# Optimization experiments

Hardware: AMD Instinct MI355X
Metric: run time of the kernel (lower is better)

## Reference

```python
import jax, jax.numpy as jnp
import numpy as np

EMBED_DIM = 1024
NUM_HEADS = 16
HEAD_DIM = EMBED_DIM // NUM_HEADS
B, N = 4, 2048
EPS = 1e-5


def rotate_half(x):
    x2d = x.reshape(x.shape[:-1] + (-1, 2))
    x1, x2 = x2d[..., 0], x2d[..., 1]
    return jnp.stack([-x2, x1], axis=-1).reshape(x.shape)


def apply_rotary_emb(freqs, t):
    return t * freqs[0] + rotate_half(t) * freqs[1]


def setup_inputs() -> dict:
    key = jax.random.key(0)
    ks = jax.random.split(key, 12)
    d = EMBED_DIM
    inp = {
        "x": jax.random.normal(ks[0], (B, N, d), jnp.float32),
        "encoding": jax.random.normal(ks[1], (2, N, HEAD_DIM), jnp.float32),
        "Wqkv_w": jax.random.normal(ks[2], (d, 3 * d), jnp.float32) * (1.0 / np.sqrt(d)),
        "Wqkv_b": jnp.zeros((3 * d,), jnp.float32),
        "out_w": jax.random.normal(ks[3], (d, d), jnp.float32) * (1.0 / np.sqrt(d)),
        "out_b": jnp.zeros((d,), jnp.float32),
        "ffn0_w": jax.random.normal(ks[4], (2 * d, 2 * d), jnp.float32) * (1.0 / np.sqrt(2 * d)),
        "ffn0_b": jnp.zeros((2 * d,), jnp.float32),
        "ln_scale": jnp.ones((2 * d,), jnp.float32),
        "ln_bias": jnp.zeros((2 * d,), jnp.float32),
        "ffn3_w": jax.random.normal(ks[5], (2 * d, d), jnp.float32) * (1.0 / np.sqrt(2 * d)),
        "ffn3_b": jnp.zeros((d,), jnp.float32),
    }
    return inp


def reference(x, encoding, Wqkv_w, Wqkv_b, out_w, out_b, ffn0_w, ffn0_b, ln_scale, ln_bias, ffn3_w, ffn3_b):
    b, n, d = x.shape
    # fused QKV projection
    qkv = jnp.einsum('bnd,de->bne', x, Wqkv_w) + Wqkv_b
    qkv = qkv.reshape(b, n, NUM_HEADS, HEAD_DIM, 3).transpose(0, 2, 1, 3, 4)  # (b,h,n,hd,3)
    q, k, v = qkv[..., 0], qkv[..., 1], qkv[..., 2]
    # RoPE (encoding broadcasts over batch/heads)
    q = apply_rotary_emb(encoding, q)
    k = apply_rotary_emb(encoding, k)
    # attention (no mask)
    scale = 1.0 / jnp.sqrt(jnp.asarray(HEAD_DIM, x.dtype))
    logits = jnp.einsum('bhqd,bhkd->bhqk', q, k) * scale
    attn = jax.nn.softmax(logits, axis=-1)
    context = jnp.einsum('bhqk,bhkd->bhqd', attn, v)
    message = context.transpose(0, 2, 1, 3).reshape(b, n, d)
    message = jnp.einsum('bnd,de->bne', message, out_w) + out_b
    # FFN: concat -> Dense -> LayerNorm -> GELU(exact) -> Dense
    h = jnp.concatenate([x, message], axis=-1)
    h = jnp.einsum('bnd,de->bne', h, ffn0_w) + ffn0_b
    mu = jnp.mean(h, axis=-1, keepdims=True)
    var = jnp.mean(jnp.square(h - mu), axis=-1, keepdims=True)
    h = (h - mu) * jax.lax.rsqrt(var + EPS) * ln_scale + ln_bias
    h = jax.nn.gelu(h, approximate=False)
    res = jnp.einsum('bnd,de->bne', h, ffn3_w) + ffn3_b
    return x + res
```

## Files before the change

### kernel.cpp

```cpp
#include <hip/hip_runtime.h>
#include <hip/hip_bf16.h>
#include <math.h>

typedef __bf16 bf16x8 __attribute__((ext_vector_type(8)));
typedef float f32x4 __attribute__((ext_vector_type(4)));

#define MFMA16(a, b, c) __builtin_amdgcn_mfma_f32_16x16x32_bf16((a), (b), (c), 0, 0, 0)

__device__ __forceinline__ void gload16(const void* g, void* l) {
  __builtin_amdgcn_global_load_lds((const __attribute__((address_space(1))) void*)g,
                                   (__attribute__((address_space(3))) void*)l, 16, 0, 0);
}

#define BARRIER asm volatile("s_barrier" ::: "memory")

__global__ __launch_bounds__(256) void transpose_bf16(const float* __restrict__ in,
                                                      int ldin,
                                                      __bf16* __restrict__ out,
                                                      int ldo) {
  __shared__ float tile[32][33];
  int n0 = blockIdx.x * 32, k0 = blockIdx.y * 32;
  int tx = threadIdx.x & 31, ty = threadIdx.x >> 5;
#pragma unroll
  for (int r = 0; r < 32; r += 8)
    tile[ty + r][tx] = in[(size_t)(k0 + ty + r) * ldin + n0 + tx];
  __syncthreads();
#pragma unroll
  for (int r = 0; r < 32; r += 8)
    out[(size_t)(n0 + ty + r) * ldo + k0 + tx] = (__bf16)tile[tx][ty + r];
}

__global__ __launch_bounds__(256) void transpose_qkv_perm(const float* __restrict__ in,
                                                          __bf16* __restrict__ out) {
  __shared__ float tile[32][33];
  int n0 = blockIdx.x * 32, k0 = blockIdx.y * 32;
  int tx = threadIdx.x & 31, ty = threadIdx.x >> 5;
#pragma unroll
  for (int r = 0; r < 32; r += 8)
    tile[ty + r][tx] = in[(size_t)(k0 + ty + r) * 3072 + n0 + tx];
  __syncthreads();
#pragma unroll
  for (int r = 0; r < 32; r += 8) {
    int n = n0 + ty + r;
    int h = n / 192, rem = n % 192, hd = rem / 3, which = rem % 3;
    int np = which * 1024 + h * 64 + hd;
    out[(size_t)np * 1024 + k0 + tx] = (__bf16)tile[tx][ty + r];
  }
}

__global__ __launch_bounds__(256) void bias_perm(const float* __restrict__ b,
                                                 float* __restrict__ bp) {
  int n = blockIdx.x * 256 + threadIdx.x;
  if (n < 3072) {
    int h = n / 192, rem = n % 192, hd = rem / 3, which = rem % 3;
    bp[which * 1024 + h * 64 + hd] = b[n];
  }
}

__global__ __launch_bounds__(256) void convert_plain(const float* __restrict__ in,
                                                     __bf16* __restrict__ out) {
  int id = blockIdx.x * 256 + threadIdx.x;
  const float* src = in + (size_t)id * 8;
  __bf16 tmp[8];
#pragma unroll
  for (int e = 0; e < 8; ++e) tmp[e] = (__bf16)src[e];
  *(uint4*)(out + (size_t)id * 8) = *(uint4*)tmp;
}

__global__ __launch_bounds__(256) void convert_x(const float* __restrict__ x,
                                                 __bf16* __restrict__ h) {
  int id = blockIdx.x * 256 + threadIdx.x;
  int row = id >> 7, cc = id & 127;
  const float* src = x + (size_t)row * 1024 + cc * 8;
  __bf16 tmp[8];
#pragma unroll
  for (int e = 0; e < 8; ++e) tmp[e] = (__bf16)src[e];
  *(uint4*)(h + (size_t)row * 2048 + cc * 8) = *(uint4*)tmp;
}

__global__ __launch_bounds__(256) void fuse_bias_part(const float* __restrict__ bout,
                                                      const float* __restrict__ w0,
                                                      float* __restrict__ part) {
  int n = blockIdx.x * 256 + threadIdx.x;
  int e0 = blockIdx.y * 64;
  float s = 0.f;
#pragma unroll 4
  for (int e = 0; e < 64; ++e)
    s += bout[e0 + e] * w0[(size_t)(1024 + e0 + e) * 2048 + n];
  part[(size_t)blockIdx.y * 2048 + n] = s;
}

__global__ __launch_bounds__(256) void fuse_bias_red(const float* __restrict__ part,
                                                     const float* __restrict__ b0,
                                                     float* __restrict__ bf) {
  int n = blockIdx.x * 256 + threadIdx.x;
  float s = b0[n];
#pragma unroll
  for (int y = 0; y < 16; ++y) s += part[(size_t)y * 2048 + n];
  bf[n] = s;
}

template <typename OutT, bool HAS_RES, bool HAS_BIAS>
__global__ __launch_bounds__(256) void gemm_kernel(
    const __bf16* __restrict__ A, int lda,
    const __bf16* __restrict__ Bt,
    const float* __restrict__ bias,
    OutT* __restrict__ C, int ldc,
    const float* __restrict__ res,
    int M, int Nn, int K) {
  __shared__ __attribute__((aligned(16))) __bf16 As[128 * 64];
  __shared__ __attribute__((aligned(16))) __bf16 Bs[128 * 64];

  const int t = threadIdx.x;
  const int row0A = blockIdx.x * 128;
  const int row0B = blockIdx.y * 128;
  const int wave = t >> 6, lane = t & 63;
  const int wm = wave >> 1, wn = wave & 1;
  const int g = lane >> 4, lr = lane & 15;

  f32x4 acc[4][4] = {};

  for (int k0 = 0; k0 < K; k0 += 64) {
#pragma unroll
    for (int p = 0; p < 4; ++p) {
      int cbase = (wave * 4 + p) * 64;
      int ci = cbase + lane;
      int r = ci >> 3, cp = ci & 7, cl = cp ^ (r & 7);
      gload16(A + (size_t)(row0A + r) * lda + k0 + cl * 8, &As[cbase * 8]);
      gload16(Bt + (size_t)(row0B + r) * K + k0 + cl * 8, &Bs[cbase * 8]);
    }
    __syncthreads();
#pragma unroll
    for (int kk = 0; kk < 2; ++kk) {
      bf16x8 af[4], bfr[4];
#pragma unroll
      for (int mt = 0; mt < 4; ++mt) {
        int r = wm * 64 + mt * 16 + lr, c = kk * 4 + g;
        af[mt] = *(const bf16x8*)((char*)As + r * 128 + ((c ^ (r & 7)) * 16));
      }
#pragma unroll
      for (int nt = 0; nt < 4; ++nt) {
        int r = wn * 64 + nt * 16 + lr, c = kk * 4 + g;
        bfr[nt] = *(const bf16x8*)((char*)Bs + r * 128 + ((c ^ (r & 7)) * 16));
      }
#pragma unroll
      for (int mt = 0; mt < 4; ++mt)
#pragma unroll
        for (int nt = 0; nt < 4; ++nt)
          acc[mt][nt] = MFMA16(af[mt], bfr[nt], acc[mt][nt]);
    }
    __syncthreads();
  }

  float bias_v[4];
#pragma unroll
  for (int nt = 0; nt < 4; ++nt)
    bias_v[nt] = HAS_BIAS ? bias[row0B + wn * 64 + nt * 16 + lr] : 0.f;
#pragma unroll
  for (int mt = 0; mt < 4; ++mt) {
    int grow_base = row0A + wm * 64 + mt * 16 + g * 4;
#pragma unroll
    for (int nt = 0; nt < 4; ++nt) {
      int gcol = row0B + wn * 64 + nt * 16 + lr;
#pragma unroll
      for (int j = 0; j < 4; ++j) {
        int grow = grow_base + j;
        float v = acc[mt][nt][j] + bias_v[nt];
        if (HAS_RES) v += res[(size_t)grow * ldc + gcol];
        C[(size_t)grow * ldc + gcol] = (OutT)v;
      }
    }
  }
}

template <typename OutT>
__global__ __launch_bounds__(512, 2) void gemm256p(
    const __bf16* __restrict__ A, int lda,
    const __bf16* __restrict__ Bt, int ldb,
    const float* __restrict__ bias,
    OutT* __restrict__ C, int ldc, int K) {
  __shared__ __attribute__((aligned(16))) __bf16 As[2][256 * 64];
  __shared__ __attribute__((aligned(16))) __bf16 Bs[2][256 * 64];

  const int t = threadIdx.x;
  const int wave = t >> 6, lane = t & 63;
  const int wm = wave >> 2, wn = wave & 3;
  const int g = lane >> 4, lr = lane & 15;
  const int row0A = blockIdx.x * 256, row0B = blockIdx.y * 256;
  const int L = K >> 6;

  f32x4 acc[8][4] = {};

#define STG_A(tile, i)                                                        \
  {                                                                           \
    int cb = ((i) * 8 + wave) * 64;                                           \
    int ci = cb + lane;                                                       \
    int r = ci >> 3, cl = (ci & 7) ^ (r & 7);                                 \
    gload16(A + (size_t)(row0A + r) * lda + (size_t)(tile) * 64 + cl * 8,     \
            &As[(tile) & 1][cb * 8]);                                         \
  }
#define STG_B(tile, i)                                                        \
  {                                                                           \
    int cb = ((i) * 8 + wave) * 64;                                           \
    int ci = cb + lane;                                                       \
    int r = ci >> 3, cl = (ci & 7) ^ (r & 7);                                 \
    gload16(Bt + (size_t)(row0B + r) * ldb + (size_t)(tile) * 64 + cl * 8,    \
            &Bs[(tile) & 1][cb * 8]);                                         \
  }
#define AFRAG(d, mi, ks)                                                      \
  (*(const bf16x8*)((const char*)As[d] + (wm * 128 + (mi) * 16 + lr) * 128 +  \
                    ((((ks) * 4 + g) ^ (lr & 7)) * 16)))
#define BFRAG(d, ni, ks)                                                      \
  (*(const bf16x8*)((const char*)Bs[d] + (wn * 64 + (ni) * 16 + lr) * 128 +   \
                    ((((ks) * 4 + g) ^ (lr & 7)) * 16)))

#pragma unroll
  for (int i = 0; i < 4; ++i) STG_A(0, i);
#pragma unroll
  for (int i = 0; i < 4; ++i) STG_B(0, i);
  STG_A(1, 0);
  STG_A(1, 1);
  asm volatile("s_waitcnt vmcnt(2)" ::: "memory");
  BARRIER;

  for (int tt = 0; tt < L; ++tt) {
    const int d = tt & 1;
    const bool s1 = (tt + 1) < L, s2 = (tt + 2) < L;
    bf16x8 aL[4][2], aH[4][2], bL[2][2], bH[2][2];

#pragma unroll
    for (int mi = 0; mi < 4; ++mi) {
      aL[mi][0] = AFRAG(d, mi, 0);
      aL[mi][1] = AFRAG(d, mi, 1);
    }
#pragma unroll
    for (int ni = 0; ni < 2; ++ni) {
      bL[ni][0] = BFRAG(d, ni, 0);
      bL[ni][1] = BFRAG(d, ni, 1);
    }
    if (s1) { STG_A(tt + 1, 2); STG_A(tt + 1, 3); }
    BARRIER;
    __builtin_amdgcn_s_setprio(1);
#pragma unroll
    for (int mi = 0; mi < 4; ++mi)
#pragma unroll
      for (int ni = 0; ni < 2; ++ni) {
        acc[mi][ni] = MFMA16(aL[mi][0], bL[ni][0], acc[mi][ni]);
        acc[mi][ni] = MFMA16(aL[mi][1], bL[ni][1], acc[mi][ni]);
      }
    __builtin_amdgcn_s_setprio(0);
    BARRIER;

#pragma unroll
    for (int ni = 0; ni < 2; ++ni) {
      bH[ni][0] = BFRAG(d, ni + 2, 0);
      bH[ni][1] = BFRAG(d, ni + 2, 1);
    }
    if (s1) { STG_B(tt + 1, 0); STG_B(tt + 1, 1); }
    BARRIER;
    __builtin_amdgcn_s_setprio(1);
#pragma unroll
    for (int mi = 0; mi < 4; ++mi)
#pragma unroll
      for (int ni = 0; ni < 2; ++ni) {
        acc[mi][ni + 2] = MFMA16(aL[mi][0], bH[ni][0], acc[mi][ni + 2]);
        acc[mi][ni + 2] = MFMA16(aL[mi][1], bH[ni][1], acc[mi][ni + 2]);
      }
    __builtin_amdgcn_s_setprio(0);
    BARRIER;

#pragma unroll
    for (int mi = 0; mi < 4; ++mi) {
      aH[mi][0] = AFRAG(d, mi + 4, 0);
      aH[mi][1] = AFRAG(d, mi + 4, 1);
    }
    if (s1) { STG_B(tt + 1, 2); STG_B(tt + 1, 3); }
    BARRIER;
    __builtin_amdgcn_s_setprio(1);
#pragma unroll
    for (int mi = 0; mi < 4; ++mi)
#pragma unroll
      for (int ni = 0; ni < 2; ++ni) {
        acc[mi + 4][ni + 2] = MFMA16(aH[mi][0], bH[ni][0], acc[mi + 4][ni + 2]);
        acc[mi + 4][ni + 2] = MFMA16(aH[mi][1], bH[ni][1], acc[mi + 4][ni + 2]);
      }
    __builtin_amdgcn_s_setprio(0);
    BARRIER;

    if (s2) { STG_A(tt + 2, 0); STG_A(tt + 2, 1); }
    __builtin_amdgcn_s_setprio(1);
#pragma unroll
    for (int mi = 0; mi < 4; ++mi)
#pragma unroll
      for (int ni = 0; ni < 2; ++ni) {
        acc[mi + 4][ni] = MFMA16(aH[mi][0], bL[ni][0], acc[mi + 4][ni]);
        acc[mi + 4][ni] = MFMA16(aH[mi][1], bL[ni][1], acc[mi + 4][ni]);
      }
    __builtin_amdgcn_s_setprio(0);
    if (s2)
      asm volatile("s_waitcnt vmcnt(2)" ::: "memory");
    else
      asm volatile("s_waitcnt vmcnt(0)" ::: "memory");
    BARRIER;
  }
#undef STG_A
#undef STG_B
#undef AFRAG
#undef BFRAG

  float bias_v[4];
#pragma unroll
  for (int ni = 0; ni < 4; ++ni) bias_v[ni] = bias[row0B + wn * 64 + ni * 16 + lr];
#pragma unroll
  for (int mi = 0; mi < 8; ++mi) {
    int grow_base = row0A + wm * 128 + mi * 16 + g * 4;
#pragma unroll
    for (int ni = 0; ni < 4; ++ni) {
      int gcol = row0B + wn * 64 + ni * 16 + lr;
#pragma unroll
      for (int j = 0; j < 4; ++j)
        C[(size_t)(grow_base + j) * ldc + gcol] = (OutT)(acc[mi][ni][j] + bias_v[ni]);
    }
  }
}

__global__ __launch_bounds__(256) void rope_scatter(
    const __bf16* __restrict__ qkv, const float* __restrict__ enc,
    __bf16* __restrict__ q, __bf16* __restrict__ kk, __bf16* __restrict__ vt) {
  int bh = blockIdx.y;
  int b = bh >> 4, h = bh & 15;
  int n0 = blockIdx.x * 64;
  int t = threadIdx.x;
  const float QSC = 0.125f * 1.44269504088896f;
#pragma unroll
  for (int i = 0; i < 2; ++i) {
    int id = t + i * 256;
    int nl = id >> 3, cc = id & 7;
    int n = n0 + nl;
    size_t row = (size_t)(b * 2048 + n) * 3072;
    bf16x8 qv = *(const bf16x8*)(qkv + row + h * 64 + cc * 8);
    bf16x8 kv = *(const bf16x8*)(qkv + row + 1024 + h * 64 + cc * 8);
    const float* e0 = enc + (size_t)n * 64 + cc * 8;
    const float* e1 = e0 + 131072;
    __bf16 qo[8], ko[8];
#pragma unroll
    for (int e = 0; e < 8; e += 2) {
      float q0 = (float)qv[e], q1 = (float)qv[e + 1];
      float k0 = (float)kv[e], k1 = (float)kv[e + 1];
      float f00 = e0[e], f01 = e0[e + 1], f10 = e1[e], f11 = e1[e + 1];
      qo[e] = (__bf16)((q0 * f00 - q1 * f10) * QSC);
      qo[e + 1] = (__bf16)((q1 * f01 + q0 * f11) * QSC);
      ko[e] = (__bf16)(k0 * f00 - k1 * f10);
      ko[e + 1] = (__bf16)(k1 * f01 + k0 * f11);
    }
    size_t qb = ((size_t)bh * 2048 + n) * 64 + cc * 8;
    *(uint4*)(q + qb) = *(uint4*)qo;
    *(uint4*)(kk + qb) = *(uint4*)ko;
  }
#pragma unroll
  for (int i = 0; i < 2; ++i) {
    int id = t + i * 256;
    int hd = id >> 3, c = id & 7;
    __bf16 tmp[8];
#pragma unroll
    for (int e = 0; e < 8; ++e) {
      int kv = (c >> 2) * 32 + (e >> 2) * 16 + (c & 3) * 4 + (e & 3);
      int n = n0 + kv;
      tmp[e] = qkv[(size_t)(b * 2048 + n) * 3072 + 2048 + h * 64 + hd];
    }
    *(uint4*)(vt + ((size_t)bh * 64 + hd) * 2048 + n0 + c * 8) = *(uint4*)tmp;
  }
}

__global__ __launch_bounds__(256) void attn_kernel(
    const __bf16* __restrict__ q, const __bf16* __restrict__ k,
    const __bf16* __restrict__ vt, __bf16* __restrict__ ctx) {
  __shared__ __attribute__((aligned(16))) __bf16 Ks[2][64 * 64];
  __shared__ __attribute__((aligned(16))) __bf16 Vs[2][64 * 64];

  int nwg = gridDim.x * gridDim.y;
  int bid0 = blockIdx.y * gridDim.x + blockIdx.x;
  int bid = (bid0 & 7) * (nwg >> 3) + (bid0 >> 3);
  const int bh = bid >> 4, qblk = bid & 15;
  const int b = bh >> 4, h = bh & 15;
  const int q0 = qblk * 128;
  const int t = threadIdx.x, wave = t >> 6, lane = t & 63;
  const int g = lane >> 4, lr = lane & 15;
  const int qrow0 = q0 + wave * 32;

  const __bf16* kbase = k + (size_t)bh * 2048 * 64;
  const __bf16* vbase = vt + (size_t)bh * 64 * 2048;

  bf16x8 qf[2][2];
#pragma unroll
  for (int u = 0; u < 2; ++u)
#pragma unroll
    for (int kc = 0; kc < 2; ++kc)
      qf[u][kc] = *(const bf16x8*)(q + ((size_t)bh * 2048 + qrow0 + u * 16 + lr) * 64 +
                                   kc * 32 + g * 8);

  bf16x8 ones;
#pragma unroll
  for (int e = 0; e < 8; ++e) ones[e] = (__bf16)1.0f;

  f32x4 o[2][4] = {};
  f32x4 lacc[2] = {};

#define STAGE_ATTN(buf, kv0)                                                    \
  {                                                                             \
    _Pragma("unroll") for (int p = 0; p < 2; ++p) {                             \
      int cbase = wave * 128 + p * 64;                                          \
      int ci = cbase + lane;                                                    \
      int r = ci >> 3, cp = ci & 7, cl = cp ^ (r & 7);                          \
      gload16(kbase + (size_t)((kv0) + r) * 64 + cl * 8, &Ks[buf][cbase * 8]);  \
      gload16(vbase + (size_t)r * 2048 + (kv0) + cl * 8, &Vs[buf][cbase * 8]);  \
    }                                                                           \
  }

  STAGE_ATTN(0, 0);
  __syncthreads();
  int buf = 0;

  for (int kv0 = 0; kv0 < 2048; kv0 += 64) {
    if (kv0 + 64 < 2048) STAGE_ATTN(buf ^ 1, kv0 + 64);

    f32x4 s[2][4];
    __builtin_amdgcn_s_setprio(1);
#pragma unroll
    for (int nt = 0; nt < 4; ++nt) {
      int r = nt * 16 + lr;
      bf16x8 kf0 = *(const bf16x8*)((char*)Ks[buf] + r * 128 + ((g ^ (r & 7)) * 16));
      bf16x8 kf1 = *(const bf16x8*)((char*)Ks[buf] + r * 128 + (((4 + g) ^ (r & 7)) * 16));
#pragma unroll
      for (int u = 0; u < 2; ++u) {
        f32x4 a = {};
        a = MFMA16(kf0, qf[u][0], a);
        a = MFMA16(kf1, qf[u][1], a);
        s[u][nt] = a;
      }
    }
    __builtin_amdgcn_s_setprio(0);

#pragma unroll
    for (int t2 = 0; t2 < 2; ++t2) {
      bf16x8 pf[2];
#pragma unroll
      for (int u = 0; u < 2; ++u) {
#pragma unroll
        for (int e = 0; e < 8; ++e)
          pf[u][e] = (__bf16)__builtin_amdgcn_exp2f(s[u][2 * t2 + (e >> 2)][e & 3]);
        lacc[u] = MFMA16(ones, pf[u], lacc[u]);
      }
      __builtin_amdgcn_s_setprio(1);
#pragma unroll
      for (int nt = 0; nt < 4; ++nt) {
        int r = nt * 16 + lr;
        bf16x8 vf = *(const bf16x8*)((char*)Vs[buf] + r * 128 + (((t2 * 4 + g) ^ (r & 7)) * 16));
#pragma unroll
        for (int u = 0; u < 2; ++u) o[u][nt] = MFMA16(vf, pf[u], o[u][nt]);
      }
      __builtin_amdgcn_s_setprio(0);
    }
    __syncthreads();
    buf ^= 1;
  }

#pragma unroll
  for (int u = 0; u < 2; ++u) {
    float inv = 1.f / lacc[u][0];
    size_t obase = ((size_t)(b * 2048 + qrow0 + u * 16 + lr)) * 2048 + 1024 + h * 64;
#pragma unroll
    for (int nt = 0; nt < 4; ++nt) {
      __bf16 w4[4];
#pragma unroll
      for (int j = 0; j < 4; ++j) w4[j] = (__bf16)(o[u][nt][j] * inv);
      *(uint2*)(ctx + obase + nt * 16 + g * 4) = *(uint2*)w4;
    }
  }
#undef STAGE_ATTN
}

__global__ __launch_bounds__(256) void ln_gelu(const __bf16* __restrict__ hin,
                                               const float* __restrict__ lns,
                                               const float* __restrict__ lnb,
                                               __bf16* __restrict__ hout) {
  int row = blockIdx.x;
  const __bf16* rp = hin + (size_t)row * 2048;
  int t = threadIdx.x;
  __bf16 tmp[8];
  *(uint4*)tmp = *(const uint4*)(rp + t * 8);
  float vals[8], s = 0.f, s2 = 0.f;
#pragma unroll
  for (int e = 0; e < 8; ++e) {
    float x = (float)tmp[e];
    vals[e] = x;
    s += x;
    s2 += x * x;
  }
#pragma unroll
  for (int m = 1; m < 64; m <<= 1) {
    s += __shfl_xor(s, m, 64);
    s2 += __shfl_xor(s2, m, 64);
  }
  __shared__ float red[8];
  int wave = t >> 6, lane = t & 63;
  if (lane == 0) { red[wave] = s; red[4 + wave] = s2; }
  __syncthreads();
  s = red[0] + red[1] + red[2] + red[3];
  s2 = red[4] + red[5] + red[6] + red[7];
  float mu = s * (1.f / 2048.f);
  float var = s2 * (1.f / 2048.f) - mu * mu;
  float rstd = rsqrtf(var + 1e-5f);
  __bf16 outv[8];
#pragma unroll
  for (int e = 0; e < 8; ++e) {
    int c = t * 8 + e;
    float xh = (vals[e] - mu) * rstd * lns[c] + lnb[c];
    float gg = 0.5f * xh * (1.f + erff(xh * 0.70710678118f));
    outv[e] = (__bf16)gg;
  }
  *(uint4*)(hout + (size_t)row * 2048 + t * 8) = *(uint4*)outv;
}

extern "C" void kernel_launch(void* const* d_in, const int* in_sizes, int n_in,
                              void* d_out, int out_size, void* d_ws, size_t ws_size,
                              hipStream_t stream) {
  const float* x = (const float*)d_in[0];
  const float* enc = (const float*)d_in[1];
  const float* wqkv = (const float*)d_in[2];
  const float* bqkv = (const float*)d_in[3];
  const float* wout = (const float*)d_in[4];
  const float* bout = (const float*)d_in[5];
  const float* wffn0 = (const float*)d_in[6];
  const float* bffn0 = (const float*)d_in[7];
  const float* lns = (const float*)d_in[8];
  const float* lnb = (const float*)d_in[9];
  const float* wffn3 = (const float*)d_in[10];
  const float* bffn3 = (const float*)d_in[11];
  float* out = (float*)d_out;
  char* ws = (char*)d_ws;

  __bf16* wT_qkv = (__bf16*)(ws + 0);
  __bf16* wT_ffn0 = (__bf16*)(ws + 6291456);
  __bf16* wT_ffn3 = (__bf16*)(ws + 14680064);
  __bf16* wout_bf = (__bf16*)(ws + 18874368);
  __bf16* w0bT = (__bf16*)(ws + 20971520);
  float* bias_part = (float*)(ws + 20971520);
  float* bqkv_p = (float*)(ws + 25165824);
  float* bffn0_f = (float*)(ws + 25178112);
  __bf16* h_in = (__bf16*)(ws + 25186304);
  __bf16* qkv = (__bf16*)(ws + 58740736);
  __bf16* ffn0o = qkv;
  __bf16* qb = (__bf16*)(ws + 109072384);
  __bf16* h2 = qb;
  __bf16* kb = (__bf16*)(ws + 125849600);
  __bf16* vtb = (__bf16*)(ws + 142626816);

  dim3 blk(256);
  transpose_qkv_perm<<<dim3(96, 32), blk, 0, stream>>>(wqkv, wT_qkv);
  bias_perm<<<12, blk, 0, stream>>>(bqkv, bqkv_p);
  transpose_bf16<<<dim3(64, 32), blk, 0, stream>>>(wffn0, 2048, wT_ffn0, 2048);
  transpose_bf16<<<dim3(64, 32), blk, 0, stream>>>(wffn0 + (size_t)1024 * 2048, 2048,
                                                   w0bT, 1024);
  transpose_bf16<<<dim3(32, 64), blk, 0, stream>>>(wffn3, 1024, wT_ffn3, 2048);
  convert_plain<<<512, blk, 0, stream>>>(wout, wout_bf);
  gemm_kernel<__bf16, false, false><<<dim3(16, 8), blk, 0, stream>>>(
      w0bT, 1024, wout_bf, nullptr, wT_ffn0 + 1024, 2048, nullptr, 2048, 1024, 1024);
  fuse_bias_part<<<dim3(8, 16), blk, 0, stream>>>(bout, wffn0, bias_part);
  fuse_bias_red<<<8, blk, 0, stream>>>(bias_part, bffn0, bffn0_f);
  convert_x<<<4096, blk, 0, stream>>>(x, h_in);

  gemm256p<__bf16><<<dim3(32, 12), dim3(512), 0, stream>>>(
      h_in, 2048, wT_qkv, 1024, bqkv_p, qkv, 3072, 1024);

  rope_scatter<<<dim3(32, 64), blk, 0, stream>>>(qkv, enc, qb, kb, vtb);
  attn_kernel<<<dim3(16, 64), blk, 0, stream>>>(qb, kb, vtb, h_in);

  gemm256p<__bf16><<<dim3(32, 8), dim3(512), 0, stream>>>(
      h_in, 2048, wT_ffn0, 2048, bffn0_f, ffn0o, 2048, 2048);

  ln_gelu<<<8192, blk, 0, stream>>>(ffn0o, lns, lnb, h2);

  gemm_kernel<float, true, true><<<dim3(64, 8), blk, 0, stream>>>(
      h2, 2048, wT_ffn3, bffn3, out, 1024, x, 8192, 1024, 2048);
}
```

Measured before the change: 393.7 us.

## Merge prep kernels into two launches and double attention query tile per wave

Ten weight/bias/input preparation kernels are collapsed into two launches (prep1 dispatching by block index, prep2 combining the wout-fold GEMM with the bias reduction). This cuts launch overhead and inter-kernel gaps, and bias_part moves to its own workspace slot so it no longer aliases w0bT. The attention kernel now handles 256 query rows per block (64 per wave), which halves the grid and reuses each staged K/V tile across twice as many queries. The cost is more registers for the o, lacc and pf accumulators, which may lower occupancy.

```diff
diff --git a/kernel.cpp b/kernel.cpp
--- a/kernel.cpp
+++ b/kernel.cpp
@@ -14,13 +14,10 @@
 
 #define BARRIER asm volatile("s_barrier" ::: "memory")
 
-__global__ __launch_bounds__(256) void transpose_bf16(const float* __restrict__ in,
-                                                      int ldin,
-                                                      __bf16* __restrict__ out,
-                                                      int ldo) {
-  __shared__ float tile[32][33];
-  int n0 = blockIdx.x * 32, k0 = blockIdx.y * 32;
-  int tx = threadIdx.x & 31, ty = threadIdx.x >> 5;
+__device__ __forceinline__ void tr_body(float (*tile)[33], const float* __restrict__ in,
+                                        int ldin, __bf16* __restrict__ out, int ldo,
+                                        int n0, int k0, int t) {
+  int tx = t & 31, ty = t >> 5;
 #pragma unroll
   for (int r = 0; r < 32; r += 8)
     tile[ty + r][tx] = in[(size_t)(k0 + ty + r) * ldin + n0 + tx];
@@ -30,74 +27,141 @@
     out[(size_t)(n0 + ty + r) * ldo + k0 + tx] = (__bf16)tile[tx][ty + r];
 }
 
-__global__ __launch_bounds__(256) void transpose_qkv_perm(const float* __restrict__ in,
-                                                          __bf16* __restrict__ out) {
+__global__ __launch_bounds__(256) void prep1(
+    const float* __restrict__ wqkv, __bf16* __restrict__ wT_qkv,
+    const float* __restrict__ wffn0, __bf16* __restrict__ wT_ffn0,
+    __bf16* __restrict__ w0bT,
+    const float* __restrict__ wffn3, __bf16* __restrict__ wT_ffn3,
+    const float* __restrict__ wout, __bf16* __restrict__ wout_bf,
+    const float* __restrict__ bqkv, float* __restrict__ bqkv_p,
+    const float* __restrict__ bout, float* __restrict__ bias_part,
+    const float* __restrict__ x, __bf16* __restrict__ h_in) {
   __shared__ float tile[32][33];
-  int n0 = blockIdx.x * 32, k0 = blockIdx.y * 32;
-  int tx = threadIdx.x & 31, ty = threadIdx.x >> 5;
-#pragma unroll
-  for (int r = 0; r < 32; r += 8)
-    tile[ty + r][tx] = in[(size_t)(k0 + ty + r) * 3072 + n0 + tx];
-  __syncthreads();
-#pragma unroll
-  for (int r = 0; r < 32; r += 8) {
-    int n = n0 + ty + r;
-    int h = n / 192, rem = n % 192, hd = rem / 3, which = rem % 3;
-    int np = which * 1024 + h * 64 + hd;
-    out[(size_t)np * 1024 + k0 + tx] = (__bf16)tile[tx][ty + r];
-  }
-}
-
-__global__ __launch_bounds__(256) void bias_perm(const float* __restrict__ b,
-                                                 float* __restrict__ bp) {
-  int n = blockIdx.x * 256 + threadIdx.x;
-  if (n < 3072) {
-    int h = n / 192, rem = n % 192, hd = rem / 3, which = rem % 3;
-    bp[which * 1024 + h * 64 + hd] = b[n];
-  }
-}
-
-__global__ __launch_bounds__(256) void convert_plain(const float* __restrict__ in,
-                                                     __bf16* __restrict__ out) {
-  int id = blockIdx.x * 256 + threadIdx.x;
-  const float* src = in + (size_t)id * 8;
-  __bf16 tmp[8];
-#pragma unroll
-  for (int e = 0; e < 8; ++e) tmp[e] = (__bf16)src[e];
-  *(uint4*)(out + (size_t)id * 8) = *(uint4*)tmp;
-}
-
-__global__ __launch_bounds__(256) void convert_x(const float* __restrict__ x,
-                                                 __bf16* __restrict__ h) {
-  int id = blockIdx.x * 256 + threadIdx.x;
-  int row = id >> 7, cc = id & 127;
-  const float* src = x + (size_t)row * 1024 + cc * 8;
-  __bf16 tmp[8];
-#pragma unroll
-  for (int e = 0; e < 8; ++e) tmp[e] = (__bf16)src[e];
-  *(uint4*)(h + (size_t)row * 2048 + cc * 8) = *(uint4*)tmp;
-}
-
-__global__ __launch_bounds__(256) void fuse_bias_part(const float* __restrict__ bout,
-                                                      const float* __restrict__ w0,
-                                                      float* __restrict__ part) {
-  int n = blockIdx.x * 256 + threadIdx.x;
-  int e0 = blockIdx.y * 64;
-  float s = 0.f;
+  const int bid = blockIdx.x;
+  const int t = threadIdx.x;
+
+  if (bid < 3072) {
+    int bx = bid % 96, by = bid / 96;
+    int n0 = bx * 32, k0 = by * 32;
+    int tx = t & 31, ty = t >> 5;
+#pragma unroll
+    for (int r = 0; r < 32; r += 8)
+      tile[ty + r][tx] = wqkv[(size_t)(k0 + ty + r) * 3072 + n0 + tx];
+    __syncthreads();
+#pragma unroll
+    for (int r = 0; r < 32; r += 8) {
+      int n = n0 + ty + r;
+      int h = n / 192, rem = n % 192, hd = rem / 3, which = rem % 3;
+      int np = which * 1024 + h * 64 + hd;
+      wT_qkv[(size_t)np * 1024 + k0 + tx] = (__bf16)tile[tx][ty + r];
+    }
+  } else if (bid < 5120) {
+    int lb = bid - 3072, bx = lb % 64, by = lb / 64;
+    tr_body(tile, wffn0, 2048, wT_ffn0, 2048, bx * 32, by * 32, t);
+  } else if (bid < 7168) {
+    int lb = bid - 5120, bx = lb % 64, by = lb / 64;
+    tr_body(tile, wffn0 + (size_t)1024 * 2048, 2048, w0bT, 1024, bx * 32, by * 32, t);
+  } else if (bid < 9216) {
+    int lb = bid - 7168, bx = lb % 32, by = lb / 32;
+    tr_body(tile, wffn3, 1024, wT_ffn3, 2048, bx * 32, by * 32, t);
+  } else if (bid < 9728) {
+    int id = (bid - 9216) * 256 + t;
+    const float* src = wout + (size_t)id * 8;
+    __bf16 tmp[8];
+#pragma unroll
+    for (int e = 0; e < 8; ++e) tmp[e] = (__bf16)src[e];
+    *(uint4*)(wout_bf + (size_t)id * 8) = *(uint4*)tmp;
+  } else if (bid < 9740) {
+    int n = (bid - 9728) * 256 + t;
+    if (n < 3072) {
+      int h = n / 192, rem = n % 192, hd = rem / 3, which = rem % 3;
+      bqkv_p[which * 1024 + h * 64 + hd] = bqkv[n];
+    }
+  } else if (bid < 9868) {
+    int lb = bid - 9740;
+    int n = (lb % 8) * 256 + t;
+    int e0 = (lb / 8) * 64;
+    float s = 0.f;
 #pragma unroll 4
-  for (int e = 0; e < 64; ++e)
-    s += bout[e0 + e] * w0[(size_t)(1024 + e0 + e) * 2048 + n];
-  part[(size_t)blockIdx.y * 2048 + n] = s;
-}
-
-__global__ __launch_bounds__(256) void fuse_bias_red(const float* __restrict__ part,
-                                                     const float* __restrict__ b0,
-                                                     float* __restrict__ bf) {
-  int n = blockIdx.x * 256 + threadIdx.x;
-  float s = b0[n];
-#pragma unroll
-  for (int y = 0; y < 16; ++y) s += part[(size_t)y * 2048 + n];
-  bf[n] = s;
+    for (int e = 0; e < 64; ++e)
+      s += bout[e0 + e] * wffn0[(size_t)(1024 + e0 + e) * 2048 + n];
+    bias_part[(size_t)(lb / 8) * 2048 + n] = s;
+  } else {
+    int id = (bid - 9868) * 256 + t;
+    int row = id >> 7, cc = id & 127;
+    const float* src = x + (size_t)row * 1024 + cc * 8;
+    __bf16 tmp[8];
+#pragma unroll
+    for (int e = 0; e < 8; ++e) tmp[e] = (__bf16)src[e];
+    *(uint4*)(h_in + (size_t)row * 2048 + cc * 8) = *(uint4*)tmp;
+  }
+}
+
+__global__ __launch_bounds__(256) void prep2(
+    const __bf16* __restrict__ w0bT, const __bf16* __restrict__ wout_bf,
+    __bf16* __restrict__ wT_ffn0,
+    const float* __restrict__ bias_part, const float* __restrict__ bffn0,
+    float* __restrict__ bffn0_f) {
+  const int bid = blockIdx.x;
+  const int t = threadIdx.x;
+  if (bid >= 128) {
+    int n = (bid - 128) * 256 + t;
+    float s = bffn0[n];
+#pragma unroll
+    for (int y = 0; y < 16; ++y) s += bias_part[(size_t)y * 2048 + n];
+    bffn0_f[n] = s;
+    return;
+  }
+  __shared__ __attribute__((aligned(16))) __bf16 As[128 * 64];
+  __shared__ __attribute__((aligned(16))) __bf16 Bs[128 * 64];
+  const int row0A = (bid % 16) * 128;
+  const int row0B = (bid / 16) * 128;
+  const int wave = t >> 6, lane = t & 63;
+  const int wm = wave >> 1, wn = wave & 1;
+  const int g = lane >> 4, lr = lane & 15;
+  f32x4 acc[4][4] = {};
+  for (int k0 = 0; k0 < 1024; k0 += 64) {
+#pragma unroll
+    for (int p = 0; p < 4; ++p) {
+      int cbase = (wave * 4 + p) * 64;
+      int ci = cbase + lane;
+      int r = ci >> 3, cp = ci & 7, cl = cp ^ (r & 7);
+      gload16(w0bT + (size_t)(row0A + r) * 1024 + k0 + cl * 8, &As[cbase * 8]);
+      gload16(wout_bf + (size_t)(row0B + r) * 1024 + k0 + cl * 8, &Bs[cbase * 8]);
+    }
+    __syncthreads();
+#pragma unroll
+    for (int kk = 0; kk < 2; ++kk) {
+      bf16x8 af[4], bfr[4];
+#pragma unroll
+      for (int mt = 0; mt < 4; ++mt) {
+        int r = wm * 64 + mt * 16 + lr, c = kk * 4 + g;
+        af[mt] = *(const bf16x8*)((char*)As + r * 128 + ((c ^ (r & 7)) * 16));
+      }
+#pragma unroll
+      for (int nt = 0; nt < 4; ++nt) {
+        int r = wn * 64 + nt * 16 + lr, c = kk * 4 + g;
+        bfr[nt] = *(const bf16x8*)((char*)Bs + r * 128 + ((c ^ (r & 7)) * 16));
+      }
+#pragma unroll
+      for (int mt = 0; mt < 4; ++mt)
+#pragma unroll
+        for (int nt = 0; nt < 4; ++nt)
+          acc[mt][nt] = MFMA16(af[mt], bfr[nt], acc[mt][nt]);
+    }
+    __syncthreads();
+  }
+#pragma unroll
+  for (int mt = 0; mt < 4; ++mt) {
+    int grow_base = row0A + wm * 64 + mt * 16 + g * 4;
+#pragma unroll
+    for (int nt = 0; nt < 4; ++nt) {
+      int gcol = row0B + wn * 64 + nt * 16 + lr;
+#pragma unroll
+      for (int j = 0; j < 4; ++j)
+        wT_ffn0[(size_t)(grow_base + j) * 2048 + 1024 + gcol] = (__bf16)acc[mt][nt][j];
+    }
+  }
 }
 
 template <typename OutT, bool HAS_RES, bool HAS_BIAS>
@@ -378,22 +442,21 @@
   __shared__ __attribute__((aligned(16))) __bf16 Ks[2][64 * 64];
   __shared__ __attribute__((aligned(16))) __bf16 Vs[2][64 * 64];
 
-  int nwg = gridDim.x * gridDim.y;
   int bid0 = blockIdx.y * gridDim.x + blockIdx.x;
-  int bid = (bid0 & 7) * (nwg >> 3) + (bid0 >> 3);
-  const int bh = bid >> 4, qblk = bid & 15;
+  int bid = (bid0 & 7) * 64 + (bid0 >> 3);
+  const int bh = bid >> 3, qblk = bid & 7;
   const int b = bh >> 4, h = bh & 15;
-  const int q0 = qblk * 128;
+  const int q0 = qblk * 256;
   const int t = threadIdx.x, wave = t >> 6, lane = t & 63;
   const int g = lane >> 4, lr = lane & 15;
-  const int qrow0 = q0 + wave * 32;
+  const int qrow0 = q0 + wave * 64;
 
   const __bf16* kbase = k + (size_t)bh * 2048 * 64;
   const __bf16* vbase = vt + (size_t)bh * 64 * 2048;
 
-  bf16x8 qf[2][2];
-#pragma unroll
-  for (int u = 0; u < 2; ++u)
+  bf16x8 qf[4][2];
+#pragma unroll
+  for (int u = 0; u < 4; ++u)
 #pragma unroll
     for (int kc = 0; kc < 2; ++kc)
       qf[u][kc] = *(const bf16x8*)(q + ((size_t)bh * 2048 + qrow0 + u * 16 + lr) * 64 +
@@ -403,8 +466,8 @@
 #pragma unroll
   for (int e = 0; e < 8; ++e) ones[e] = (__bf16)1.0f;
 
-  f32x4 o[2][4] = {};
-  f32x4 lacc[2] = {};
+  f32x4 o[4][4] = {};
+  f32x4 lacc[4] = {};
 
 #define STAGE_ATTN(buf, kv0)                                                    \
   {                                                                             \
@@ -424,49 +487,56 @@
   for (int kv0 = 0; kv0 < 2048; kv0 += 64) {
     if (kv0 + 64 < 2048) STAGE_ATTN(buf ^ 1, kv0 + 64);
 
-    f32x4 s[2][4];
-    __builtin_amdgcn_s_setprio(1);
+    bf16x8 kf[4][2];
 #pragma unroll
     for (int nt = 0; nt < 4; ++nt) {
       int r = nt * 16 + lr;
-      bf16x8 kf0 = *(const bf16x8*)((char*)Ks[buf] + r * 128 + ((g ^ (r & 7)) * 16));
-      bf16x8 kf1 = *(const bf16x8*)((char*)Ks[buf] + r * 128 + (((4 + g) ^ (r & 7)) * 16));
-#pragma unroll
-      for (int u = 0; u < 2; ++u) {
+      kf[nt][0] = *(const bf16x8*)((char*)Ks[buf] + r * 128 + ((g ^ (r & 7)) * 16));
+      kf[nt][1] = *(const bf16x8*)((char*)Ks[buf] + r * 128 + (((4 + g) ^ (r & 7)) * 16));
+    }
+
+    bf16x8 pf[4][2];
+#pragma unroll
+    for (int u = 0; u < 4; ++u) {
+      f32x4 s[4];
+      __builtin_amdgcn_s_setprio(1);
+#pragma unroll
+      for (int nt = 0; nt < 4; ++nt) {
         f32x4 a = {};
-        a = MFMA16(kf0, qf[u][0], a);
-        a = MFMA16(kf1, qf[u][1], a);
-        s[u][nt] = a;
-      }
-    }
-    __builtin_amdgcn_s_setprio(0);
-
-#pragma unroll
-    for (int t2 = 0; t2 < 2; ++t2) {
-      bf16x8 pf[2];
-#pragma unroll
-      for (int u = 0; u < 2; ++u) {
+        a = MFMA16(kf[nt][0], qf[u][0], a);
+        a = MFMA16(kf[nt][1], qf[u][1], a);
+        s[nt] = a;
+      }
+      __builtin_amdgcn_s_setprio(0);
+#pragma unroll
+      for (int t2 = 0; t2 < 2; ++t2)
 #pragma unroll
         for (int e = 0; e < 8; ++e)
-          pf[u][e] = (__bf16)__builtin_amdgcn_exp2f(s[u][2 * t2 + (e >> 2)][e & 3]);
-        lacc[u] = MFMA16(ones, pf[u], lacc[u]);
-      }
-      __builtin_amdgcn_s_setprio(1);
+          pf[u][t2][e] = (__bf16)__builtin_amdgcn_exp2f(s[2 * t2 + (e >> 2)][e & 3]);
+    }
+
+    __builtin_amdgcn_s_setprio(1);
+#pragma unroll
+    for (int u = 0; u < 4; ++u) {
+      lacc[u] = MFMA16(ones, pf[u][0], lacc[u]);
+      lacc[u] = MFMA16(ones, pf[u][1], lacc[u]);
+    }
+#pragma unroll
+    for (int t2 = 0; t2 < 2; ++t2)
 #pragma unroll
       for (int nt = 0; nt < 4; ++nt) {
         int r = nt * 16 + lr;
         bf16x8 vf = *(const bf16x8*)((char*)Vs[buf] + r * 128 + (((t2 * 4 + g) ^ (r & 7)) * 16));
 #pragma unroll
-        for (int u = 0; u < 2; ++u) o[u][nt] = MFMA16(vf, pf[u], o[u][nt]);
-      }
-      __builtin_amdgcn_s_setprio(0);
-    }
+        for (int u = 0; u < 4; ++u) o[u][nt] = MFMA16(vf, pf[u][t2], o[u][nt]);
+      }
+    __builtin_amdgcn_s_setprio(0);
     __syncthreads();
     buf ^= 1;
   }
 
 #pragma unroll
-  for (int u = 0; u < 2; ++u) {
+  for (int u = 0; u < 4; ++u) {
     float inv = 1.f / lacc[u][0];
     size_t obase = ((size_t)(b * 2048 + qrow0 + u * 16 + lr)) * 2048 + 1024 + h * 64;
 #pragma unroll
@@ -545,36 +615,27 @@
   __bf16* wT_ffn3 = (__bf16*)(ws + 14680064);
   __bf16* wout_bf = (__bf16*)(ws + 18874368);
   __bf16* w0bT = (__bf16*)(ws + 20971520);
-  float* bias_part = (float*)(ws + 20971520);
-  float* bqkv_p = (float*)(ws + 25165824);
-  float* bffn0_f = (float*)(ws + 25178112);
-  __bf16* h_in = (__bf16*)(ws + 25186304);
-  __bf16* qkv = (__bf16*)(ws + 58740736);
+  float* bias_part = (float*)(ws + 25165824);
+  float* bqkv_p = (float*)(ws + 25296896);
+  float* bffn0_f = (float*)(ws + 25309184);
+  __bf16* h_in = (__bf16*)(ws + 25317376);
+  __bf16* qkv = (__bf16*)(ws + 58871808);
   __bf16* ffn0o = qkv;
-  __bf16* qb = (__bf16*)(ws + 109072384);
+  __bf16* qb = (__bf16*)(ws + 109203456);
   __bf16* h2 = qb;
-  __bf16* kb = (__bf16*)(ws + 125849600);
-  __bf16* vtb = (__bf16*)(ws + 142626816);
+  __bf16* kb = (__bf16*)(ws + 125980672);
+  __bf16* vtb = (__bf16*)(ws + 142757888);
 
   dim3 blk(256);
-  transpose_qkv_perm<<<dim3(96, 32), blk, 0, stream>>>(wqkv, wT_qkv);
-  bias_perm<<<12, blk, 0, stream>>>(bqkv, bqkv_p);
-  transpose_bf16<<<dim3(64, 32), blk, 0, stream>>>(wffn0, 2048, wT_ffn0, 2048);
-  transpose_bf16<<<dim3(64, 32), blk, 0, stream>>>(wffn0 + (size_t)1024 * 2048, 2048,
-                                                   w0bT, 1024);
-  transpose_bf16<<<dim3(32, 64), blk, 0, stream>>>(wffn3, 1024, wT_ffn3, 2048);
-  convert_plain<<<512, blk, 0, stream>>>(wout, wout_bf);
-  gemm_kernel<__bf16, false, false><<<dim3(16, 8), blk, 0, stream>>>(
-      w0bT, 1024, wout_bf, nullptr, wT_ffn0 + 1024, 2048, nullptr, 2048, 1024, 1024);
-  fuse_bias_part<<<dim3(8, 16), blk, 0, stream>>>(bout, wffn0, bias_part);
-  fuse_bias_red<<<8, blk, 0, stream>>>(bias_part, bffn0, bffn0_f);
-  convert_x<<<4096, blk, 0, stream>>>(x, h_in);
+  prep1<<<13964, blk, 0, stream>>>(wqkv, wT_qkv, wffn0, wT_ffn0, w0bT, wffn3, wT_ffn3,
+                                   wout, wout_bf, bqkv, bqkv_p, bout, bias_part, x, h_in);
+  prep2<<<136, blk, 0, stream>>>(w0bT, wout_bf, wT_ffn0, bias_part, bffn0, bffn0_f);
 
   gemm256p<__bf16><<<dim3(32, 12), dim3(512), 0, stream>>>(
       h_in, 2048, wT_qkv, 1024, bqkv_p, qkv, 3072, 1024);
 
   rope_scatter<<<dim3(32, 64), blk, 0, stream>>>(qkv, enc, qb, kb, vtb);
-  attn_kernel<<<dim3(16, 64), blk, 0, stream>>>(qb, kb, vtb, h_in);
+  attn_kernel<<<dim3(8, 64), blk, 0, stream>>>(qb, kb, vtb, h_in);
 
   gemm256p<__bf16><<<dim3(32, 8), dim3(512), 0, stream>>>(
       h_in, 2048, wT_ffn0, 2048, bffn0_f, ffn0o, 2048, 2048);
```

Measured after the change: 372.5 us. 5.4% less time.
